# Performance work log

Hardware: AMD Instinct MI355X
Metric: run time of the kernel (lower is better)

## Reference

```python
import jax, jax.numpy as jnp
import numpy as np

B, O, A, H, Z = 4096, 512, 64, 2048, 256
CLAMP = 10.0


def _lin(x, w, b):
    # torch nn.Linear layout: w [out, in]
    return x @ w.T + b


def setup_inputs() -> dict:
    key = jax.random.key(0)
    ks = jax.random.split(key, 24)
    n = jax.random.normal
    s = 0.02
    inp = {
        'x_t': n(ks[0], (B, O), jnp.float32),
        'a_prev': n(ks[1], (B, A), jnp.float32),
        'h_prev': n(ks[2], (B, H), jnp.float32),
        'eps': n(ks[3], (B, Z), jnp.float32),
        # prior_net: Linear(H,H) -> ReLU -> Linear(H, 2Z)
        'prior_w1': n(ks[4], (H, H), jnp.float32) * s,
        'prior_b1': jnp.zeros((H,), jnp.float32),
        'prior_w2': n(ks[5], (2 * Z, H), jnp.float32) * s,
        'prior_b2': jnp.zeros((2 * Z,), jnp.float32),
        # enc_net: Linear(O+H,H) -> ReLU -> Linear(H, 2Z)
        'enc_w1': n(ks[6], (H, O + H), jnp.float32) * s,
        'enc_b1': jnp.zeros((H,), jnp.float32),
        'enc_w2': n(ks[7], (2 * Z, H), jnp.float32) * s,
        'enc_b2': jnp.zeros((2 * Z,), jnp.float32),
        # dec_net: Linear(Z+H,H) -> ReLU -> Linear(H, 2O)
        'dec_w1': n(ks[8], (H, Z + H), jnp.float32) * s,
        'dec_b1': jnp.zeros((H,), jnp.float32),
        'dec_w2': n(ks[9], (2 * O, H), jnp.float32) * s,
        'dec_b2': jnp.zeros((2 * O,), jnp.float32),
        # GRUCell: input = O + A + Z, gates ordered (r, z, n)
        'w_ih': n(ks[10], (3 * H, O + A + Z), jnp.float32) * s,
        'w_hh': n(ks[11], (3 * H, H), jnp.float32) * s,
        'b_ih': jnp.zeros((3 * H,), jnp.float32),
        'b_hh': jnp.zeros((3 * H,), jnp.float32),
    }
    return inp


def vrnn_step(x_t, a_prev, h_prev, eps,
              prior_w1, prior_b1, prior_w2, prior_b2,
              enc_w1, enc_b1, enc_w2, enc_b2,
              dec_w1, dec_b1, dec_w2, dec_b2,
              w_ih, w_hh, b_ih, b_hh):
    # prior stats from h_prev
    prior_stats = _lin(jax.nn.relu(_lin(h_prev, prior_w1, prior_b1)), prior_w2, prior_b2)
    mu_p, logvar_p = jnp.split(prior_stats, 2, axis=-1)

    # encoder on [x, h]
    enc_stats = _lin(jax.nn.relu(_lin(jnp.concatenate([x_t, h_prev], -1), enc_w1, enc_b1)), enc_w2, enc_b2)
    mu_q, logvar_q = jnp.split(enc_stats, 2, axis=-1)
    logvar_q = jnp.clip(logvar_q, -CLAMP, CLAMP)
    std_q = jnp.exp(0.5 * logvar_q)
    z_t = mu_q + eps * std_q  # reparameterization

    # decoder on [z, h]
    dec_out = _lin(jax.nn.relu(_lin(jnp.concatenate([z_t, h_prev], -1), dec_w1, dec_b1)), dec_w2, dec_b2)
    mu_x, logvar_x = jnp.split(dec_out, 2, axis=-1)
    logvar_x = jnp.clip(logvar_x, -CLAMP, CLAMP)
    nll = 0.5 * jnp.sum((x_t - mu_x) ** 2 * jnp.exp(-logvar_x) + logvar_x, axis=-1)

    # KL(q || p), diagonal Gaussians
    var_p = jnp.exp(logvar_p)
    kl = 0.5 * jnp.sum((mu_q - mu_p) ** 2 / var_p + jnp.exp(logvar_q) / var_p
                       + (logvar_p - logvar_q) - 1.0, axis=-1)

    # GRUCell (torch gate order: r, z, n)
    rnn_in = jnp.concatenate([x_t, z_t, a_prev], -1)
    gi = rnn_in @ w_ih.T + b_ih
    gh = h_prev @ w_hh.T + b_hh
    i_r, i_z, i_n = jnp.split(gi, 3, axis=-1)
    h_r, h_z, h_n = jnp.split(gh, 3, axis=-1)
    r = jax.nn.sigmoid(i_r + h_r)
    zg = jax.nn.sigmoid(i_z + h_z)
    n = jnp.tanh(i_n + r * h_n)
    h_t = (1.0 - zg) * n + zg * h_prev

    return h_t, nll, kl, z_t, mu_q, logvar_q


def reference(x_t, a_prev, h_prev, eps,
              prior_w1, prior_b1, prior_w2, prior_b2,
              enc_w1, enc_b1, enc_w2, enc_b2,
              dec_w1, dec_b1, dec_w2, dec_b2,
              w_ih, w_hh, b_ih, b_hh):
    return vrnn_step(x_t, a_prev, h_prev, eps,
                     prior_w1, prior_b1, prior_w2, prior_b2,
                     enc_w1, enc_b1, enc_w2, enc_b2,
                     dec_w1, dec_b1, dec_w2, dec_b2,
                     w_ih, w_hh, b_ih, b_hh)
```

## Files before the change

### kernel.cpp

```cpp
#include <hip/hip_runtime.h>
#include <stdint.h>


#define B_SZ 4096
#define H_SZ 2048
#define Z_SZ 256

typedef __attribute__((ext_vector_type(4))) float f32x4;
typedef __attribute__((ext_vector_type(8))) short s16x8;

__device__ __forceinline__ uint16_t f2b(float f) {
  union { float f; uint32_t u; } v; v.f = f;
  uint32_t u = v.u;
  uint32_t r = (u + 0x7FFFu + ((u >> 16) & 1u)) >> 16;
  return (uint16_t)r;
}
__device__ __forceinline__ float b2f(uint16_t h) {
  union { uint32_t u; float f; } v; v.u = ((uint32_t)h) << 16; return v.f;
}
__device__ __forceinline__ float clip10(float v) { return fminf(fmaxf(v, -10.0f), 10.0f); }

struct MC {
  const float* src[14];
  uint16_t* dst[14];
  int c8[14];
  int sld[14];
  int dld[14];
  int base[15];
};

__global__ __launch_bounds__(256) void multiconv(MC mc, int nseg, int total) {
  int gid = blockIdx.x * 256 + threadIdx.x;
  if (gid >= total) return;
  int s = 0;
  while (s + 1 < nseg && gid >= mc.base[s + 1]) ++s;
  int local = gid - mc.base[s];
  int c8 = mc.c8[s];
  int row = local / c8;
  int cg = local - row * c8;
  const f32x4* sp = (const f32x4*)(mc.src[s] + (size_t)row * mc.sld[s] + (size_t)cg * 8);
  f32x4 lo = sp[0], hi = sp[1];
  s16x8 p;
  p[0] = (short)f2b(lo[0]); p[1] = (short)f2b(lo[1]);
  p[2] = (short)f2b(lo[2]); p[3] = (short)f2b(lo[3]);
  p[4] = (short)f2b(hi[0]); p[5] = (short)f2b(hi[1]);
  p[6] = (short)f2b(hi[2]); p[7] = (short)f2b(hi[3]);
  *(s16x8*)(mc.dst[s] + (size_t)row * mc.dld[s] + (size_t)cg * 8) = p;
}

__global__ void biascat_kernel(const float* __restrict__ b0, const float* __restrict__ b1,
                               const float* __restrict__ b2, const float* __restrict__ b3,
                               float* __restrict__ dst) {
  int j = blockIdx.x * 256 + threadIdx.x;
  float v;
  if (j < 2048) v = b0[j];
  else if (j < 8192) v = b1[j - 2048];
  else if (j < 10240) v = b2[j - 8192];
  else v = b3[j - 10240];
  dst[j] = v;
}

__device__ __forceinline__ void gload_lds16(const uint16_t* g, uint16_t* l) {
  __builtin_amdgcn_global_load_lds(
      (const __attribute__((address_space(1))) uint32_t*)g,
      (__attribute__((address_space(3))) uint32_t*)(uintptr_t)(void*)l,
      16, 0, 0);
}

__global__ __launch_bounds__(512, 2)
void gemm8p(const uint16_t* __restrict__ A, int lda,
            const uint16_t* __restrict__ W,
            const float* __restrict__ bias,
            uint16_t* __restrict__ C, int ldc, int splitN,
            int Nt, int K) {
  __shared__ uint16_t Ab[2][2][8192];
  __shared__ uint16_t Bb[2][2][8192];
  const int NT = K >> 6;
  int mtile = blockIdx.x / Nt;
  int ntile = blockIdx.x - mtile * Nt;
  const int brow = mtile << 8, bcol = ntile << 8;
  const int tid = threadIdx.x;
  const int l = tid & 63;
  const int w = tid >> 6;
  const int wr = w >> 2, wcn = w & 3;
  const int fr = l & 15, fq = l >> 4;
  const int sr0 = tid >> 3;
  const int scg = tid & 7;
  const int dstoff = tid * 8;

  f32x4 acc[8][4] = {};

  auto stage_half = [&](int t, int q, int d) {
#pragma unroll
    for (int r = 0; r < 2; ++r) {
      int row = r * 64 + sr0;
      int col = (scg ^ (row & 7)) << 3;
      if (q < 2)
        gload_lds16(A + (size_t)(brow + q * 128 + row) * lda + t * 64 + col,
                    &Ab[d][q][r * 4096 + dstoff]);
      else
        gload_lds16(W + (size_t)(bcol + (q - 2) * 128 + row) * K + t * 64 + col,
                    &Bb[d][q - 2][r * 4096 + dstoff]);
    }
  };

#pragma unroll
  for (int q = 0; q < 4; ++q) stage_half(0, q, 0);

  for (int t = 0; t < NT; ++t) {
    const int d = t & 1;
    const bool more = (t + 1 < NT);
    if (more) {
      stage_half(t + 1, 0, d ^ 1);
      asm volatile("s_waitcnt vmcnt(2)" ::: "memory");
    } else {
      asm volatile("s_waitcnt vmcnt(0)" ::: "memory");
    }
    __builtin_amdgcn_s_barrier();

#pragma unroll
    for (int q = 0; q < 4; ++q) {
      const int mh = q >> 1, nh = q & 1;
      if (q > 0 && more) stage_half(t + 1, q, d ^ 1);
      s16x8 fb[2][2];
#pragma unroll
      for (int nn = 0; nn < 2; ++nn)
#pragma unroll
        for (int ks = 0; ks < 2; ++ks) {
          int row = wcn * 64 + nh * 32 + nn * 16 + fr;
          int half = row >> 7, rl = row & 127;
          fb[nn][ks] = *(const s16x8*)&Bb[d][half]
              [rl * 64 + ((ks * 32 + fq * 8) ^ ((rl & 7) << 3))];
        }
      s16x8 fa[4][2];
#pragma unroll
      for (int mm = 0; mm < 4; ++mm)
#pragma unroll
        for (int ks = 0; ks < 2; ++ks) {
          int rl = mh * 64 + mm * 16 + fr;
          fa[mm][ks] = *(const s16x8*)&Ab[d][wr]
              [rl * 64 + ((ks * 32 + fq * 8) ^ ((rl & 7) << 3))];
        }
      __builtin_amdgcn_s_setprio(1);
#pragma unroll
      for (int mm = 0; mm < 4; ++mm)
#pragma unroll
        for (int nn = 0; nn < 2; ++nn)
#pragma unroll
          for (int ks = 0; ks < 2; ++ks)
            acc[mh * 4 + mm][nh * 2 + nn] = __builtin_amdgcn_mfma_f32_16x16x32_bf16(
                fa[mm][ks], fb[nn][ks], acc[mh * 4 + mm][nh * 2 + nn], 0, 0, 0);
      __builtin_amdgcn_s_setprio(0);
      __builtin_amdgcn_s_barrier();
    }
  }

#pragma unroll
  for (int m = 0; m < 8; ++m) {
    int grow = brow + wr * 128 + m * 16 + fq * 4;
#pragma unroll
    for (int n = 0; n < 4; ++n) {
      int gcol = bcol + wcn * 64 + n * 16 + fr;
      float bs = bias[gcol];
      bool doRelu = gcol < splitN;
#pragma unroll
      for (int i = 0; i < 4; ++i) {
        float v = acc[m][n][i] + bs;
        if (doRelu) v = fmaxf(v, 0.0f);
        C[(size_t)(grow + i) * ldc + gcol] = f2b(v);
      }
    }
  }
}

template <int EPI>
__global__ __launch_bounds__(256)
void gemm_bt(const uint16_t* __restrict__ A0, int lda0, int ks1,
             const uint16_t* __restrict__ A1, int lda1, int ks2,
             const uint16_t* __restrict__ A2, int lda2,
             const uint16_t* __restrict__ W,
             const float* __restrict__ bias0, const float* __restrict__ bias1,
             uint16_t* __restrict__ C0, int ldc0, int splitN,
             uint16_t* __restrict__ C1, int ldc1,
             int Nt, int K) {
  __shared__ uint16_t As[128 * 64];
  __shared__ uint16_t Ws[128 * 64];
  int mtile = blockIdx.x / Nt;
  int ntile = blockIdx.x - mtile * Nt;
  const int row0 = mtile << 7, col0 = ntile << 7;
  const int t = threadIdx.x;
  const int w = t >> 6, l = t & 63;
  const int wr = w >> 1, wc = w & 1;
  const int sr = l >> 3, scg = l & 7;
  const int fr = l & 15, fq = l >> 4;

  f32x4 acc[4][4] = {};

  const uint16_t* Wbase = W + (size_t)(col0 + w * 32 + sr) * K + scg * 8;

  for (int k0 = 0; k0 < K; k0 += 64) {
    const uint16_t* ab; int ald, koff;
    if (k0 < ks1)      { ab = A0; ald = lda0; koff = k0; }
    else if (k0 < ks2) { ab = A1; ald = lda1; koff = k0 - ks1; }
    else               { ab = A2; ald = lda2; koff = k0 - ks2; }
    const uint16_t* Abase = ab + (size_t)(row0 + w * 32 + sr) * ald + koff + scg * 8;
#pragma unroll
    for (int j = 0; j < 4; ++j)
      gload_lds16(Abase + (size_t)(j * 8) * ald, &As[(w * 32 + j * 8) * 64]);
#pragma unroll
    for (int j = 0; j < 4; ++j)
      gload_lds16(Wbase + (size_t)(j * 8) * K + k0, &Ws[(w * 32 + j * 8) * 64]);
    __syncthreads();
#pragma unroll
    for (int ks = 0; ks < 2; ++ks) {
      s16x8 fa[4], fb[4];
#pragma unroll
      for (int m = 0; m < 4; ++m)
        fa[m] = *(const s16x8*)&As[(wr * 64 + m * 16 + fr) * 64 + ks * 32 + fq * 8];
#pragma unroll
      for (int n = 0; n < 4; ++n)
        fb[n] = *(const s16x8*)&Ws[(wc * 64 + n * 16 + fr) * 64 + ks * 32 + fq * 8];
#pragma unroll
      for (int m = 0; m < 4; ++m)
#pragma unroll
        for (int n = 0; n < 4; ++n)
          acc[m][n] = __builtin_amdgcn_mfma_f32_16x16x32_bf16(fa[m], fb[n], acc[m][n], 0, 0, 0);
    }
    __syncthreads();
  }

#pragma unroll
  for (int m = 0; m < 4; ++m) {
    int grow = row0 + wr * 64 + m * 16 + fq * 4;
#pragma unroll
    for (int n = 0; n < 4; ++n) {
      int gcol = col0 + wc * 64 + n * 16 + fr;
      bool first = (EPI != 3) || (gcol < splitN);
      float bs = first ? bias0[gcol] : bias1[gcol - splitN];
#pragma unroll
      for (int i = 0; i < 4; ++i) {
        size_t idx0 = (size_t)(grow + i) * ldc0 + gcol;
        if (EPI == 6) {
          float v6 = acc[m][n][i] + b2f(C0[idx0]);
          C0[idx0] = f2b(fmaxf(v6, 0.0f));
        } else {
          float v = acc[m][n][i] + bs;
          if (EPI == 1 || (EPI == 3 && first)) v = fmaxf(v, 0.0f);
          if (first)
            C0[idx0] = f2b(v);
          else
            C1[(size_t)(grow + i) * ldc1 + (gcol - splitN)] = f2b(v);
        }
      }
    }
  }
}

__global__ __launch_bounds__(256)
void gemm_ks(const uint16_t* __restrict__ A, int lda,
             const uint16_t* __restrict__ W, int Wld,
             float* __restrict__ P, int N,
             int Nt, int Khalf) {
  __shared__ uint16_t As[128 * 64];
  __shared__ uint16_t Ws[128 * 64];
  int bg = gridDim.x >> 1;
  int half = blockIdx.x >= bg;
  int bid = blockIdx.x - half * bg;
  int mtile = bid / Nt;
  int ntile = bid - mtile * Nt;
  const int row0 = mtile << 7, col0 = ntile << 7;
  const int t = threadIdx.x;
  const int w = t >> 6, l = t & 63;
  const int wr = w >> 1, wc = w & 1;
  const int sr = l >> 3, scg = l & 7;
  const int fr = l & 15, fq = l >> 4;

  f32x4 acc[4][4] = {};

  const uint16_t* Ab = A + half * Khalf;
  const uint16_t* Wb = W + half * Khalf;
  const uint16_t* Wbase = Wb + (size_t)(col0 + w * 32 + sr) * Wld + scg * 8;
  const uint16_t* Abase0 = Ab + (size_t)(row0 + w * 32 + sr) * lda + scg * 8;

  for (int k0 = 0; k0 < Khalf; k0 += 64) {
#pragma unroll
    for (int j = 0; j < 4; ++j)
      gload_lds16(Abase0 + (size_t)(j * 8) * lda + k0, &As[(w * 32 + j * 8) * 64]);
#pragma unroll
    for (int j = 0; j < 4; ++j)
      gload_lds16(Wbase + (size_t)(j * 8) * Wld + k0, &Ws[(w * 32 + j * 8) * 64]);
    __syncthreads();
#pragma unroll
    for (int ks = 0; ks < 2; ++ks) {
      s16x8 fa[4], fb[4];
#pragma unroll
      for (int m = 0; m < 4; ++m)
        fa[m] = *(const s16x8*)&As[(wr * 64 + m * 16 + fr) * 64 + ks * 32 + fq * 8];
#pragma unroll
      for (int n = 0; n < 4; ++n)
        fb[n] = *(const s16x8*)&Ws[(wc * 64 + n * 16 + fr) * 64 + ks * 32 + fq * 8];
#pragma unroll
      for (int m = 0; m < 4; ++m)
#pragma unroll
        for (int n = 0; n < 4; ++n)
          acc[m][n] = __builtin_amdgcn_mfma_f32_16x16x32_bf16(fa[m], fb[n], acc[m][n], 0, 0, 0);
    }
    __syncthreads();
  }

  float* Pf = P + (size_t)half * B_SZ * N;
#pragma unroll
  for (int m = 0; m < 4; ++m) {
    int grow = row0 + wr * 64 + m * 16 + fq * 4;
#pragma unroll
    for (int n = 0; n < 4; ++n) {
      int gcol = col0 + wc * 64 + n * 16 + fr;
#pragma unroll
      for (int i = 0; i < 4; ++i)
        Pf[(size_t)(grow + i) * N + gcol] = acc[m][n][i];
    }
  }
}

__global__ __launch_bounds__(256)
void combine2(const float* __restrict__ P, const float* __restrict__ bias,
              uint16_t* __restrict__ dst, int N, int total4) {
  int i = blockIdx.x * 256 + threadIdx.x;
  if (i >= total4) return;
  size_t idx = (size_t)i * 4;
  const float* P1 = P + (size_t)B_SZ * N;
  f32x4 a = *(const f32x4*)(P + idx);
  f32x4 b = *(const f32x4*)(P1 + idx);
  int col = (int)(idx & (size_t)(N - 1));
#pragma unroll
  for (int k = 0; k < 4; ++k)
    dst[idx + k] = f2b(a[k] + b[k] + bias[col + k]);
}

__global__ void z_kernel_t1(const uint16_t* __restrict__ es, const float* __restrict__ eps,
                            float* __restrict__ oz, float* __restrict__ omu,
                            float* __restrict__ olq, uint16_t* __restrict__ zbuf) {
  int i = blockIdx.x * 256 + threadIdx.x;
  int b = i >> 8, j = i & 255;
  float mu = b2f(es[(size_t)b * 512 + j]);
  float lq = clip10(b2f(es[(size_t)b * 512 + 256 + j]));
  float z = mu + eps[i] * __expf(0.5f * lq);
  oz[i] = z; omu[i] = mu; olq[i] = lq;
  zbuf[i] = f2b(z);
}

__device__ __forceinline__ float block_sum256(float v) {
  __shared__ float ps[4];
#pragma unroll
  for (int o = 32; o > 0; o >>= 1) v += __shfl_xor(v, o, 64);
  int l = threadIdx.x & 63, w = threadIdx.x >> 6;
  if (l == 0) ps[w] = v;
  __syncthreads();
  float r = ps[0] + ps[1] + ps[2] + ps[3];
  __syncthreads();
  return r;
}

__global__ __launch_bounds__(256)
void gru_fused_t1(const uint16_t* __restrict__ gi, int ldgi,
                  const uint16_t* __restrict__ gh, int ldgh,
                  const float* __restrict__ hp, const float* __restrict__ x,
                  const uint16_t* __restrict__ dec, const uint16_t* __restrict__ pst,
                  const uint16_t* __restrict__ es,
                  float* __restrict__ out_h, float* __restrict__ out_nll,
                  float* __restrict__ out_kl) {
  int b = blockIdx.x, t = threadIdx.x;
  size_t gbi = (size_t)b * ldgi + (size_t)t * 8;
  size_t gbh = (size_t)b * ldgh + (size_t)t * 8;
  s16x8 ir = *(const s16x8*)(gi + gbi);
  s16x8 iz = *(const s16x8*)(gi + gbi + 2048);
  s16x8 inn = *(const s16x8*)(gi + gbi + 4096);
  s16x8 hr = *(const s16x8*)(gh + gbh);
  s16x8 hz = *(const s16x8*)(gh + gbh + 2048);
  s16x8 hn = *(const s16x8*)(gh + gbh + 4096);
  size_t hbase = (size_t)b * 2048 + (size_t)t * 8;
  f32x4 h0 = *(const f32x4*)(hp + hbase);
  f32x4 h1v = *(const f32x4*)(hp + hbase + 4);
  f32x4 o0, o1;
#pragma unroll
  for (int e = 0; e < 8; ++e) {
    float r = 1.f / (1.f + __expf(-(b2f((uint16_t)ir[e]) + b2f((uint16_t)hr[e]))));
    float zg = 1.f / (1.f + __expf(-(b2f((uint16_t)iz[e]) + b2f((uint16_t)hz[e]))));
    float nv = b2f((uint16_t)inn[e]) + r * b2f((uint16_t)hn[e]);
    float t2 = __expf(-2.f * fabsf(nv));
    float n = (1.f - t2) / (1.f + t2);
    n = (nv >= 0.f) ? n : -n;
    float hv = (e < 4) ? h0[e] : h1v[e - 4];
    float o = (1.f - zg) * n + zg * hv;
    if (e < 4) o0[e] = o; else o1[e - 4] = o;
  }
  *(f32x4*)(out_h + hbase) = o0;
  *(f32x4*)(out_h + hbase + 4) = o1;

  float s = 0.f;
#pragma unroll
  for (int rr = 0; rr < 2; ++rr) {
    int j = t + rr * 256;
    float mu = b2f(dec[(size_t)b * 1024 + j]);
    float lx = clip10(b2f(dec[(size_t)b * 1024 + 512 + j]));
    float d = x[(size_t)b * 512 + j] - mu;
    s += d * d * __expf(-lx) + lx;
  }
  s = block_sum256(s);
  if (t == 0) out_nll[b] = 0.5f * s;

  float mu_p = b2f(pst[(size_t)b * 512 + t]);
  float lp = b2f(pst[(size_t)b * 512 + 256 + t]);
  float mu_q = b2f(es[(size_t)b * 512 + t]);
  float lq = clip10(b2f(es[(size_t)b * 512 + 256 + t]));
  float dq = mu_q - mu_p;
  float enl = __expf(-lp);
  float kv = dq * dq * enl + __expf(lq) * enl + (lp - lq) - 1.0f;
  kv = block_sum256(kv);
  if (t == 0) out_kl[b] = 0.5f * kv;
}

template <int MODE>
__global__ __launch_bounds__(256)
void gemm_nv(const float* __restrict__ A0, int ld0, int s1,
             const float* __restrict__ A1, int ld1, int s2,
             const float* __restrict__ A2, int ld2,
             const float* __restrict__ W, const float* __restrict__ bias,
             float* __restrict__ C, int N, int K) {
  int nb = N >> 8;
  int m = blockIdx.x / nb;
  int n = (blockIdx.x - m * nb) * 256 + threadIdx.x;
  const float* w = W + (size_t)n * K;
  float acc = 0.f;
  int k = 0;
  for (; k < s1; ++k) acc += A0[(size_t)m * ld0 + k] * w[k];
  for (; k < s2; ++k) acc += A1[(size_t)m * ld1 + (k - s1)] * w[k];
  for (; k < K; ++k) acc += A2[(size_t)m * ld2 + (k - s2)] * w[k];
  acc += bias[n];
  if (MODE == 1) acc = fmaxf(acc, 0.f);
  C[(size_t)m * N + n] = acc;
}

__global__ void z_nv(const float* __restrict__ ests, const float* __restrict__ eps,
                     float* __restrict__ oz, float* __restrict__ omu,
                     float* __restrict__ olq, float* __restrict__ zs, int row0, int nR) {
  int i = blockIdx.x * 256 + threadIdx.x;
  if (i >= nR * 256) return;
  int bl = i >> 8, j = i & 255;
  size_t g = (size_t)(row0 + bl) * 256 + j;
  float mu = ests[(size_t)bl * 512 + j];
  float lq = clip10(ests[(size_t)bl * 512 + 256 + j]);
  float z = mu + eps[g] * __expf(0.5f * lq);
  oz[g] = z; omu[g] = mu; olq[g] = lq;
  zs[(size_t)bl * 256 + j] = z;
}

__global__ void nll_nv(const float* __restrict__ x, const float* __restrict__ decs,
                       float* __restrict__ out, int row0) {
  int bl = blockIdx.x, l = threadIdx.x;
  int gb = row0 + bl;
  float s = 0.f;
  for (int j = l; j < 512; j += 64) {
    float mu = decs[(size_t)bl * 1024 + j];
    float lx = clip10(decs[(size_t)bl * 1024 + 512 + j]);
    float d = x[(size_t)gb * 512 + j] - mu;
    s += d * d * __expf(-lx) + lx;
  }
#pragma unroll
  for (int o = 32; o > 0; o >>= 1) s += __shfl_xor(s, o, 64);
  if (l == 0) out[gb] = 0.5f * s;
}

__global__ void kl_nv(const float* __restrict__ psts, const float* __restrict__ ests,
                      float* __restrict__ out, int row0) {
  int bl = blockIdx.x, l = threadIdx.x;
  int gb = row0 + bl;
  float s = 0.f;
  for (int j = l; j < 256; j += 64) {
    float mu_p = psts[(size_t)bl * 512 + j];
    float lp = psts[(size_t)bl * 512 + 256 + j];
    float mu_q = ests[(size_t)bl * 512 + j];
    float lq = clip10(ests[(size_t)bl * 512 + 256 + j]);
    float d = mu_q - mu_p;
    float enl = __expf(-lp);
    s += d * d * enl + __expf(lq) * enl + (lp - lq) - 1.0f;
  }
#pragma unroll
  for (int o = 32; o > 0; o >>= 1) s += __shfl_xor(s, o, 64);
  if (l == 0) out[gb] = 0.5f * s;
}

__global__ void gru_nv(const float* __restrict__ gis, const float* __restrict__ ghs,
                       const float* __restrict__ hp, float* __restrict__ ho,
                       int row0, int nR) {
  int i = blockIdx.x * 256 + threadIdx.x;
  if (i >= nR * 2048) return;
  int bl = i >> 11, j = i & 2047;
  size_t lb = (size_t)bl * 6144 + j;
  float r = 1.f / (1.f + __expf(-(gis[lb] + ghs[lb])));
  float zg = 1.f / (1.f + __expf(-(gis[lb + 2048] + ghs[lb + 2048])));
  float nv = gis[lb + 4096] + r * ghs[lb + 4096];
  float t2 = __expf(-2.f * fabsf(nv));
  float n = (1.f - t2) / (1.f + t2);
  n = (nv >= 0.f) ? n : -n;
  size_t g = (size_t)(row0 + bl) * 2048 + j;
  ho[g] = (1.f - zg) * n + zg * hp[g];
}

extern "C" void kernel_launch(void* const* d_in, const int* in_sizes, int n_in,
                              void* d_out, int out_size, void* d_ws, size_t ws_size,
                              hipStream_t stream) {
  const float* x_t = (const float*)d_in[0];
  const float* a_prev = (const float*)d_in[1];
  const float* h_prev = (const float*)d_in[2];
  const float* eps = (const float*)d_in[3];
  const float* prior_w1 = (const float*)d_in[4];
  const float* prior_b1 = (const float*)d_in[5];
  const float* prior_w2 = (const float*)d_in[6];
  const float* prior_b2 = (const float*)d_in[7];
  const float* enc_w1 = (const float*)d_in[8];
  const float* enc_b1 = (const float*)d_in[9];
  const float* enc_w2 = (const float*)d_in[10];
  const float* enc_b2 = (const float*)d_in[11];
  const float* dec_w1 = (const float*)d_in[12];
  const float* dec_b1 = (const float*)d_in[13];
  const float* dec_w2 = (const float*)d_in[14];
  const float* dec_b2 = (const float*)d_in[15];
  const float* w_ih = (const float*)d_in[16];
  const float* w_hh = (const float*)d_in[17];
  const float* b_ih = (const float*)d_in[18];
  const float* b_hh = (const float*)d_in[19];

  float* out = (float*)d_out;
  float* out_h = out;
  float* out_nll = out + (size_t)B_SZ * H_SZ;
  float* out_kl = out_nll + B_SZ;
  float* out_z = out_kl + B_SZ;
  float* out_mu = out_z + (size_t)B_SZ * Z_SZ;
  float* out_lq = out_mu + (size_t)B_SZ * Z_SZ;

  char* ws = (char*)d_ws;
  size_t off = 0;
  auto alloc = [&](size_t bytes) {
    void* p = ws + off;
    off += (bytes + 255) & ~(size_t)255;
    return p;
  };

  const size_t T1_DEMAND = 194297856;

  if (ws_size >= T1_DEMAND) {
    uint16_t* wmega = (uint16_t*)alloc((size_t)12288 * 2048 * 2);
    uint16_t* wih = (uint16_t*)alloc((size_t)6144 * 832 * 2);
    uint16_t* wx_enc = (uint16_t*)alloc((size_t)2048 * 512 * 2);
    uint16_t* wz_dec = (uint16_t*)alloc((size_t)2048 * 256 * 2);
    uint16_t* pw2 = (uint16_t*)alloc((size_t)512 * 2048 * 2);
    uint16_t* ew2 = (uint16_t*)alloc((size_t)512 * 2048 * 2);
    uint16_t* dw2 = (uint16_t*)alloc((size_t)1024 * 2048 * 2);
    uint16_t* xbuf = (uint16_t*)alloc((size_t)B_SZ * 512 * 2);
    uint16_t* hbuf = (uint16_t*)alloc((size_t)B_SZ * 2048 * 2);
    uint16_t* abuf = (uint16_t*)alloc((size_t)B_SZ * 64 * 2);
    uint16_t* megaC = (uint16_t*)alloc((size_t)B_SZ * 12288 * 2);
    float* biascat = (float*)alloc(12288 * 4);
    float* Pbuf = (float*)wmega;
    uint16_t* gi = wmega;
    uint16_t* pstats = hbuf;
    uint16_t* estats = hbuf + (size_t)2097152;
    uint16_t* zbuf = hbuf + (size_t)4194304;
    uint16_t* decout = pw2;

    MC mc;
    int nseg = 0, acc = 0;
    auto seg = [&](const float* s, uint16_t* d, int R, int C, int sld, int dld) {
      mc.src[nseg] = s; mc.dst[nseg] = d; mc.c8[nseg] = C / 8;
      mc.sld[nseg] = sld; mc.dld[nseg] = dld; mc.base[nseg] = acc;
      acc += R * (C / 8); ++nseg;
    };
    seg(prior_w1, wmega, 2048, 2048, 2048, 2048);
    seg(w_hh, wmega + (size_t)2048 * 2048, 6144, 2048, 2048, 2048);
    seg(enc_w1 + 512, wmega + (size_t)8192 * 2048, 2048, 2048, 2560, 2048);
    seg(dec_w1 + 256, wmega + (size_t)10240 * 2048, 2048, 2048, 2304, 2048);
    seg(enc_w1, wx_enc, 2048, 512, 2560, 512);
    seg(dec_w1, wz_dec, 2048, 256, 2304, 256);
    seg(prior_w2, pw2, 512, 2048, 2048, 2048);
    seg(enc_w2, ew2, 512, 2048, 2048, 2048);
    seg(dec_w2, dw2, 1024, 2048, 2048, 2048);
    seg(w_ih, wih, 6144, 832, 832, 832);
    seg(x_t, xbuf, B_SZ, 512, 512, 512);
    seg(h_prev, hbuf, B_SZ, 2048, 2048, 2048);
    seg(a_prev, abuf, B_SZ, 64, 64, 64);
    mc.base[nseg] = acc;
    multiconv<<<dim3((acc + 255) / 256), dim3(256), 0, stream>>>(mc, nseg, acc);
    biascat_kernel<<<dim3(48), dim3(256), 0, stream>>>(prior_b1, b_hh, enc_b1, dec_b1, biascat);

    gemm8p<<<dim3((B_SZ / 256) * 48), dim3(512), 0, stream>>>(
        hbuf, 2048, wmega, biascat, megaC, 12288, 2048, 48, 2048);
    gemm_ks<<<dim3((B_SZ / 128) * 4 * 2), dim3(256), 0, stream>>>(
        megaC, 12288, pw2, 2048, Pbuf, 512, 4, 1024);
    combine2<<<dim3(B_SZ * 512 / 4 / 256), dim3(256), 0, stream>>>(
        Pbuf, prior_b2, pstats, 512, B_SZ * 512 / 4);
    gemm_bt<6><<<dim3((B_SZ / 128) * 16), dim3(256), 0, stream>>>(
        xbuf, 512, 512, xbuf, 512, 512, xbuf, 512, wx_enc,
        enc_b1, enc_b1, megaC + 8192, 12288, 2048, megaC + 8192, 12288, 16, 512);
    gemm_ks<<<dim3((B_SZ / 128) * 4 * 2), dim3(256), 0, stream>>>(
        megaC + 8192, 12288, ew2, 2048, Pbuf, 512, 4, 1024);
    combine2<<<dim3(B_SZ * 512 / 4 / 256), dim3(256), 0, stream>>>(
        Pbuf, enc_b2, estats, 512, B_SZ * 512 / 4);
    z_kernel_t1<<<dim3(B_SZ * Z_SZ / 256), dim3(256), 0, stream>>>(
        estats, eps, out_z, out_mu, out_lq, zbuf);
    gemm_bt<6><<<dim3((B_SZ / 128) * 16), dim3(256), 0, stream>>>(
        zbuf, 256, 256, zbuf, 256, 256, zbuf, 256, wz_dec,
        dec_b1, dec_b1, megaC + 10240, 12288, 2048, megaC + 10240, 12288, 16, 256);
    gemm_ks<<<dim3((B_SZ / 128) * 8 * 2), dim3(256), 0, stream>>>(
        megaC + 10240, 12288, dw2, 2048, Pbuf, 1024, 8, 1024);
    combine2<<<dim3(B_SZ * 1024 / 4 / 256), dim3(256), 0, stream>>>(
        Pbuf, dec_b2, decout, 1024, B_SZ * 1024 / 4);
    gemm_bt<2><<<dim3((B_SZ / 128) * 48), dim3(256), 0, stream>>>(
        xbuf, 512, 512, zbuf, 256, 768, abuf, 64, wih,
        b_ih, b_ih, gi, 6144, 6144, gi, 6144, 48, 832);
    gru_fused_t1<<<dim3(B_SZ), dim3(256), 0, stream>>>(
        gi, 6144, megaC + 2048, 12288, h_prev, x_t, decout, pstats, estats,
        out_h, out_nll, out_kl);
  } else {
    int R = 512;
    while (R > 32 && (size_t)R * 66560 + 4096 > ws_size) R >>= 1;
    float* h1s = (float*)alloc((size_t)R * 2048 * 4);
    float* psts = (float*)alloc((size_t)R * 512 * 4);
    float* ests = (float*)alloc((size_t)R * 512 * 4);
    float* decs = (float*)alloc((size_t)R * 1024 * 4);
    float* zs = (float*)alloc((size_t)R * 256 * 4);
    float* gis = (float*)alloc((size_t)R * 6144 * 4);
    float* ghs = (float*)alloc((size_t)R * 6144 * 4);
    const float* dummy = x_t;

    auto nv = [&](const float* A0, int ld0, int s1, const float* A1, int ld1, int s2,
                  const float* A2, int ld2, const float* W, const float* bias,
                  float* C, int M, int N, int K, int relu) {
      dim3 grid(M * (N / 256));
      if (relu)
        gemm_nv<1><<<grid, dim3(256), 0, stream>>>(A0, ld0, s1, A1, ld1, s2, A2, ld2, W, bias, C, N, K);
      else
        gemm_nv<0><<<grid, dim3(256), 0, stream>>>(A0, ld0, s1, A1, ld1, s2, A2, ld2, W, bias, C, N, K);
    };

    for (int s = 0; s < B_SZ / R; ++s) {
      int r0 = s * R;
      const float* xs = x_t + (size_t)r0 * 512;
      const float* hs = h_prev + (size_t)r0 * 2048;
      const float* as = a_prev + (size_t)r0 * 64;
      nv(hs, 2048, 2048, dummy, 0, 2048, dummy, 0, prior_w1, prior_b1, h1s, R, 2048, 2048, 1);
      nv(h1s, 2048, 2048, dummy, 0, 2048, dummy, 0, prior_w2, prior_b2, psts, R, 512, 2048, 0);
      nv(xs, 512, 512, hs, 2048, 2560, dummy, 0, enc_w1, enc_b1, h1s, R, 2048, 2560, 1);
      nv(h1s, 2048, 2048, dummy, 0, 2048, dummy, 0, enc_w2, enc_b2, ests, R, 512, 2048, 0);
      z_nv<<<dim3((R * 256 + 255) / 256), dim3(256), 0, stream>>>(
          ests, eps, out_z, out_mu, out_lq, zs, r0, R);
      nv(zs, 256, 256, hs, 2048, 2304, dummy, 0, dec_w1, dec_b1, h1s, R, 2048, 2304, 1);
      nv(h1s, 2048, 2048, dummy, 0, 2048, dummy, 0, dec_w2, dec_b2, decs, R, 1024, 2048, 0);
      nv(hs, 2048, 2048, dummy, 0, 2048, dummy, 0, w_hh, b_hh, ghs, R, 6144, 2048, 0);
      nv(xs, 512, 512, zs, 256, 768, as, 64, w_ih, b_ih, gis, R, 6144, 832, 0);
      nll_nv<<<dim3(R), dim3(64), 0, stream>>>(x_t, decs, out_nll, r0);
      kl_nv<<<dim3(R), dim3(64), 0, stream>>>(psts, ests, out_kl, r0);
      gru_nv<<<dim3((R * 2048 + 255) / 256), dim3(256), 0, stream>>>(
          gis, ghs, h_prev, out_h, r0, R);
    }
  }
}
```

Measured before the change: 483.4 us.

## Pack x,z,a into one activation buffer, fuse combine with z sampling, use gemm8p for GRU input

Lays out x_t, z_t and a_prev contiguously in one bf16 [B,832] buffer so the GRU input projection can run as a single-operand GEMM using the larger gemm8p kernel instead of a three-source gemm_bt. It also fuses the encoder split-K combine with z sampling, removing one launch and a round trip through estats. The risk is that gemm8p's tiling, with N=6144 in 24 column blocks and K=832, may not match its assumptions, and the 832 row stride may affect how well loads align.

```diff
diff --git a/kernel.cpp b/kernel.cpp
--- a/kernel.cpp
+++ b/kernel.cpp
@@ -337,16 +337,25 @@
     dst[idx + k] = f2b(a[k] + b[k] + bias[col + k]);
 }
 
-__global__ void z_kernel_t1(const uint16_t* __restrict__ es, const float* __restrict__ eps,
-                            float* __restrict__ oz, float* __restrict__ omu,
-                            float* __restrict__ olq, uint16_t* __restrict__ zbuf) {
+__global__ __launch_bounds__(256)
+void combine2z(const float* __restrict__ P, const float* __restrict__ bias,
+               const float* __restrict__ eps,
+               uint16_t* __restrict__ estats,
+               float* __restrict__ oz, float* __restrict__ omu, float* __restrict__ olq,
+               uint16_t* __restrict__ xza) {
   int i = blockIdx.x * 256 + threadIdx.x;
   int b = i >> 8, j = i & 255;
-  float mu = b2f(es[(size_t)b * 512 + j]);
-  float lq = clip10(b2f(es[(size_t)b * 512 + 256 + j]));
-  float z = mu + eps[i] * __expf(0.5f * lq);
-  oz[i] = z; omu[i] = mu; olq[i] = lq;
-  zbuf[i] = f2b(z);
+  const float* P1 = P + (size_t)B_SZ * 512;
+  size_t i0 = (size_t)b * 512 + j;
+  size_t i1 = i0 + 256;
+  float mu = P[i0] + P1[i0] + bias[j];
+  float lq = P[i1] + P1[i1] + bias[j + 256];
+  estats[i0] = f2b(mu);
+  estats[i1] = f2b(lq);
+  float lqc = clip10(lq);
+  float z = mu + eps[i] * __expf(0.5f * lqc);
+  oz[i] = z; omu[i] = mu; olq[i] = lqc;
+  xza[(size_t)b * 832 + 512 + j] = f2b(z);
 }
 
 __device__ __forceinline__ float block_sum256(float v) {
@@ -547,7 +556,7 @@
     return p;
   };
 
-  const size_t T1_DEMAND = 194297856;
+  const size_t T1_DEMAND = 196500000;
 
   if (ws_size >= T1_DEMAND) {
     uint16_t* wmega = (uint16_t*)alloc((size_t)12288 * 2048 * 2);
@@ -557,16 +566,14 @@
     uint16_t* pw2 = (uint16_t*)alloc((size_t)512 * 2048 * 2);
     uint16_t* ew2 = (uint16_t*)alloc((size_t)512 * 2048 * 2);
     uint16_t* dw2 = (uint16_t*)alloc((size_t)1024 * 2048 * 2);
-    uint16_t* xbuf = (uint16_t*)alloc((size_t)B_SZ * 512 * 2);
+    uint16_t* xza = (uint16_t*)alloc((size_t)B_SZ * 832 * 2);
     uint16_t* hbuf = (uint16_t*)alloc((size_t)B_SZ * 2048 * 2);
-    uint16_t* abuf = (uint16_t*)alloc((size_t)B_SZ * 64 * 2);
     uint16_t* megaC = (uint16_t*)alloc((size_t)B_SZ * 12288 * 2);
     float* biascat = (float*)alloc(12288 * 4);
     float* Pbuf = (float*)wmega;
     uint16_t* gi = wmega;
     uint16_t* pstats = hbuf;
     uint16_t* estats = hbuf + (size_t)2097152;
-    uint16_t* zbuf = hbuf + (size_t)4194304;
     uint16_t* decout = pw2;
 
     MC mc;
@@ -586,9 +593,9 @@
     seg(enc_w2, ew2, 512, 2048, 2048, 2048);
     seg(dec_w2, dw2, 1024, 2048, 2048, 2048);
     seg(w_ih, wih, 6144, 832, 832, 832);
-    seg(x_t, xbuf, B_SZ, 512, 512, 512);
+    seg(x_t, xza, B_SZ, 512, 512, 832);
+    seg(a_prev, xza + 768, B_SZ, 64, 64, 832);
     seg(h_prev, hbuf, B_SZ, 2048, 2048, 2048);
-    seg(a_prev, abuf, B_SZ, 64, 64, 64);
     mc.base[nseg] = acc;
     multiconv<<<dim3((acc + 255) / 256), dim3(256), 0, stream>>>(mc, nseg, acc);
     biascat_kernel<<<dim3(48), dim3(256), 0, stream>>>(prior_b1, b_hh, enc_b1, dec_b1, biascat);
@@ -600,24 +607,21 @@
     combine2<<<dim3(B_SZ * 512 / 4 / 256), dim3(256), 0, stream>>>(
         Pbuf, prior_b2, pstats, 512, B_SZ * 512 / 4);
     gemm_bt<6><<<dim3((B_SZ / 128) * 16), dim3(256), 0, stream>>>(
-        xbuf, 512, 512, xbuf, 512, 512, xbuf, 512, wx_enc,
+        xza, 832, 512, xza, 832, 512, xza, 832, wx_enc,
         enc_b1, enc_b1, megaC + 8192, 12288, 2048, megaC + 8192, 12288, 16, 512);
     gemm_ks<<<dim3((B_SZ / 128) * 4 * 2), dim3(256), 0, stream>>>(
         megaC + 8192, 12288, ew2, 2048, Pbuf, 512, 4, 1024);
-    combine2<<<dim3(B_SZ * 512 / 4 / 256), dim3(256), 0, stream>>>(
-        Pbuf, enc_b2, estats, 512, B_SZ * 512 / 4);
-    z_kernel_t1<<<dim3(B_SZ * Z_SZ / 256), dim3(256), 0, stream>>>(
-        estats, eps, out_z, out_mu, out_lq, zbuf);
+    combine2z<<<dim3(B_SZ * Z_SZ / 256), dim3(256), 0, stream>>>(
+        Pbuf, enc_b2, eps, estats, out_z, out_mu, out_lq, xza);
     gemm_bt<6><<<dim3((B_SZ / 128) * 16), dim3(256), 0, stream>>>(
-        zbuf, 256, 256, zbuf, 256, 256, zbuf, 256, wz_dec,
+        xza + 512, 832, 256, xza + 512, 832, 256, xza + 512, 832, wz_dec,
         dec_b1, dec_b1, megaC + 10240, 12288, 2048, megaC + 10240, 12288, 16, 256);
     gemm_ks<<<dim3((B_SZ / 128) * 8 * 2), dim3(256), 0, stream>>>(
         megaC + 10240, 12288, dw2, 2048, Pbuf, 1024, 8, 1024);
     combine2<<<dim3(B_SZ * 1024 / 4 / 256), dim3(256), 0, stream>>>(
         Pbuf, dec_b2, decout, 1024, B_SZ * 1024 / 4);
-    gemm_bt<2><<<dim3((B_SZ / 128) * 48), dim3(256), 0, stream>>>(
-        xbuf, 512, 512, zbuf, 256, 768, abuf, 64, wih,
-        b_ih, b_ih, gi, 6144, 6144, gi, 6144, 48, 832);
+    gemm8p<<<dim3((B_SZ / 256) * 24), dim3(512), 0, stream>>>(
+        xza, 832, wih, b_ih, gi, 6144, 0, 24, 832);
     gru_fused_t1<<<dim3(B_SZ), dim3(256), 0, stream>>>(
         gi, 6144, megaC + 2048, 12288, h_prev, x_t, decout, pstats, estats,
         out_h, out_nll, out_kl);
```

Measured after the change: 490.7 us. About the same (+1.5%).
